# Optimization experiments

Hardware: AMD Instinct MI355X
Metric: run time of the kernel (lower is better)

The kernel has to match this reference:

```python
import jax, jax.numpy as jnp
import numpy as np

H = 8          # heads
D = 512        # d_model
DK = D // H    # per-head dim
FF = 2048      # feed-forward size
STACKS = 3
VOCAB = 5000
PAD = 0
LN_EPS = 1e-6


def _layer_norm(x, g, b):
    mu = jnp.mean(x, axis=-1, keepdims=True)
    var = jnp.mean(jnp.square(x - mu), axis=-1, keepdims=True)
    return (x - mu) * jax.lax.rsqrt(var + LN_EPS) * g + b


def _positional_encoding(T, d):
    pos = jnp.arange(T, dtype=jnp.float32)[:, None]                      # (T,1)
    div = jnp.exp(jnp.arange(0, d, 2, dtype=jnp.float32) * (-np.log(10000.0) / d))
    pe = jnp.zeros((T, d), dtype=jnp.float32)
    pe = pe.at[:, 0::2].set(jnp.sin(pos * div))
    pe = pe.at[:, 1::2].set(jnp.cos(pos * div))
    return pe  # (T, D)


def _mha(q_in, kv, wq, bq, wk, bk, wv, bv, wo, bo, mask):
    B, Tq, _ = q_in.shape
    Tk = kv.shape[1]
    q = (q_in @ wq + bq).reshape(B, Tq, H, DK).transpose(0, 2, 1, 3)   # (B,H,Tq,DK)
    k = (kv @ wk + bk).reshape(B, Tk, H, DK).transpose(0, 2, 1, 3)
    v = (kv @ wv + bv).reshape(B, Tk, H, DK).transpose(0, 2, 1, 3)
    score = jnp.einsum('bhqd,bhkd->bhqk', q, k) / jnp.sqrt(jnp.float32(DK))
    if mask is not None:
        score = jnp.where(mask, score, jnp.float32(-1e9))
    p = jax.nn.softmax(score, axis=-1)
    out = jnp.einsum('bhqk,bhkd->bhqd', p, v)
    out = out.transpose(0, 2, 1, 3).reshape(B, Tq, D)
    return out @ wo + bo


def setup_inputs() -> dict:
    key = jax.random.key(0)
    ks = jax.random.split(key, 24)
    s = 0.02
    inp = {
        'target': jax.random.randint(ks[0], (32, 256), 0, VOCAB),
        'memory': jax.random.normal(ks[1], (32, 1024, D), dtype=jnp.float32),
        'emb': jax.random.normal(ks[2], (VOCAB, D), dtype=jnp.float32) * s,
        'ln_g': jnp.ones((D,), jnp.float32),
        'ln_b': jnp.zeros((D,), jnp.float32),
        'ff_w1': jax.random.normal(ks[3], (D, FF), jnp.float32) * s,
        'ff_b1': jnp.zeros((FF,), jnp.float32),
        'ff_w2': jax.random.normal(ks[4], (FF, D), jnp.float32) * s,
        'ff_b2': jnp.zeros((D,), jnp.float32),
    }
    names = ['wq', 'wk', 'wv', 'wo']
    for i, n in enumerate(names):
        inp['sa_' + n] = jax.random.normal(ks[5 + i], (D, D), jnp.float32) * s
        inp['sa_b' + n[1]] = jnp.zeros((D,), jnp.float32)
        inp['ca_' + n] = jax.random.normal(ks[9 + i], (D, D), jnp.float32) * s
        inp['ca_b' + n[1]] = jnp.zeros((D,), jnp.float32)
    return inp


def reference(target, memory, emb, ln_g, ln_b, ff_w1, ff_b1, ff_w2, ff_b2,
              sa_wq, sa_bq, sa_wk, sa_bk, sa_wv, sa_bv, sa_wo, sa_bo,
              ca_wq, ca_bq, ca_wk, ca_bk, ca_wv, ca_bv, ca_wo, ca_bo):
    B, T = target.shape
    x = emb[target] * jnp.sqrt(jnp.float32(D))              # (B,T,D)
    x = x + _positional_encoding(T, D)                       # dropout = identity (eval)
    # masks: causal & pad for self-attn; cross-attn mask is all-ones -> skip
    pad = (target != PAD)[:, None, :, None]                  # (B,1,T,1)
    causal = jnp.tril(jnp.ones((T, T), dtype=bool))          # (T,T)
    tgt_mask = pad & causal                                  # (B,1,T,T)
    out = x
    for _ in range(STACKS):  # shared parameters
        n = _layer_norm(out, ln_g, ln_b)
        out = out + _mha(n, n, sa_wq, sa_bq, sa_wk, sa_bk, sa_wv, sa_bv, sa_wo, sa_bo, tgt_mask)
        n = _layer_norm(out, ln_g, ln_b)
        out = out + _mha(n, memory, ca_wq, ca_bq, ca_wk, ca_bk, ca_wv, ca_bv, ca_wo, ca_bo, None)
        n = _layer_norm(out, ln_g, ln_b)
        out = out + (jax.nn.relu(n @ ff_w1 + ff_b1) @ ff_w2 + ff_b2)
    return _layer_norm(out, ln_g, ln_b)
```

## Files before the change

### kernel.cpp

```cpp
#include <hip/hip_runtime.h>
#include <cstdint>
#include <cstddef>

typedef unsigned short u16;
typedef __bf16 bf16x8 __attribute__((ext_vector_type(8)));
typedef float f32x4 __attribute__((ext_vector_type(4)));

#define DEV static __device__ __forceinline__

#define QSCALE 0.18033688011112042f

DEV u16 f2bf(float f) { unsigned v; __builtin_memcpy(&v, &f, 4); v += 0x7fffu + ((v >> 16) & 1u); return (u16)(v >> 16); }

DEV void gll16(const void* g, void* l) {
    __builtin_amdgcn_global_load_lds(
        (__attribute__((address_space(1))) void*)g,
        (__attribute__((address_space(3))) void*)l, 16, 0, 0);
}

__global__ void embed_pe(const int* __restrict__ tgt, const float* __restrict__ emb,
                         float* __restrict__ x)
{
    const int bt = blockIdx.x;
    const int t  = bt & 255;
    const int tok = tgt[bt];
    for (int d = threadIdx.x; d < 512; d += 256) {
        float e  = emb[(size_t)tok * 512 + d] * 22.62741699796952f;
        int   d0 = d & ~1;
        float ang = (float)t * expf((float)d0 * (-9.210340371976184f / 512.f));
        float pe  = (d & 1) ? cosf(ang) : sinf(ang);
        x[(size_t)bt * 512 + d] = e + pe;
    }
}

__global__ void transpose_k(const float* __restrict__ in, u16* __restrict__ out,
                            int K, int N)
{
    int id = blockIdx.x * 256 + threadIdx.x;
    int k = id / N, n = id % N;
    out[(size_t)n * K + k] = f2bf(in[id]);
}

__global__ void memcast(const float* __restrict__ in, u16* __restrict__ out)
{
    int i = (blockIdx.x * 256 + threadIdx.x) * 4;
    float4 v = *(const float4*)(in + i);
    uint2 w;
    w.x = (unsigned)f2bf(v.x) | ((unsigned)f2bf(v.y) << 16);
    w.y = (unsigned)f2bf(v.z) | ((unsigned)f2bf(v.w) << 16);
    *(uint2*)(out + i) = w;
}

__global__ void concat_bias(const float* __restrict__ a, const float* __restrict__ b,
                            float* __restrict__ out)
{
    int i = blockIdx.x * 256 + threadIdx.x;
    if (i < 512) { out[i] = a[i]; out[512 + i] = b[i]; }
}

template<bool OUTF32>
__global__ void layernorm_k(const float* __restrict__ x, const float* __restrict__ g,
                            const float* __restrict__ b, void* __restrict__ outv)
{
    const int row  = blockIdx.x * 4 + (threadIdx.x >> 6);
    const int lane = threadIdx.x & 63;
    const float* xr = x + (size_t)row * 512;
    float4 v0 = *(const float4*)(xr + lane * 4);
    float4 v1 = *(const float4*)(xr + 256 + lane * 4);
    float s = v0.x + v0.y + v0.z + v0.w + v1.x + v1.y + v1.z + v1.w;
    float q = v0.x*v0.x + v0.y*v0.y + v0.z*v0.z + v0.w*v0.w
            + v1.x*v1.x + v1.y*v1.y + v1.z*v1.z + v1.w*v1.w;
#pragma unroll
    for (int o = 1; o < 64; o <<= 1) { s += __shfl_xor(s, o, 64); q += __shfl_xor(q, o, 64); }
    float mu  = s * (1.f / 512.f);
    float var = q * (1.f / 512.f) - mu * mu;
    float rs  = rsqrtf(fmaxf(var, 0.f) + 1e-6f);

#pragma unroll
    for (int h = 0; h < 2; h++) {
        const int d0 = h * 256 + lane * 4;
        float4 v = h ? v1 : v0;
        float4 gg = *(const float4*)(g + d0);
        float4 bb = *(const float4*)(b + d0);
        float o0 = (v.x - mu) * rs * gg.x + bb.x;
        float o1 = (v.y - mu) * rs * gg.y + bb.y;
        float o2 = (v.z - mu) * rs * gg.z + bb.z;
        float o3 = (v.w - mu) * rs * gg.w + bb.w;
        if (OUTF32) {
            *(float4*)((float*)outv + (size_t)row * 512 + d0) = make_float4(o0, o1, o2, o3);
        } else {
            uint2 w;
            w.x = (unsigned)f2bf(o0) | ((unsigned)f2bf(o1) << 16);
            w.y = (unsigned)f2bf(o2) | ((unsigned)f2bf(o3) << 16);
            *(uint2*)((u16*)outv + (size_t)row * 512 + d0) = w;
        }
    }
}

template<int EPI, bool BROW, int BN, int QS>
__launch_bounds__(256, BN == 64 ? 4 : 2)
__global__ void gemm_bt(const u16* __restrict__ A, int lda,
                        const u16* __restrict__ Bt,
                        const float* __restrict__ bias,
                        void* __restrict__ outp, int ldo, int K)
{
    constexpr int NJ = BN / 32;
    __shared__ u16 As[128 * 32];
    __shared__ u16 Bs[BN * 32];
    const int tid  = threadIdx.x;
    const int lane = tid & 63;
    const int wave = tid >> 6;
    const int quad = lane >> 4, l16 = lane & 15;
    const int l4 = lane >> 2, c8 = (lane & 3) * 8;
    const int m0 = blockIdx.y * 128, n0 = blockIdx.x * BN;
    const int wm = (wave >> 1) * 64, wn = (wave & 1) * (BN / 2);

    f32x4 acc[4][NJ];
#pragma unroll
    for (int i = 0; i < 4; i++)
#pragma unroll
        for (int j = 0; j < NJ; j++) acc[i][j] = f32x4{0.f, 0.f, 0.f, 0.f};

    for (int k0 = 0; k0 < K; k0 += 32) {
        __syncthreads();
        gll16(&A[(size_t)(m0 + wave * 32 + l4)      * lda + k0 + c8], &As[(wave * 32) * 32]);
        gll16(&A[(size_t)(m0 + wave * 32 + 16 + l4) * lda + k0 + c8], &As[(wave * 32 + 16) * 32]);
        if (BN == 128) {
            gll16(&Bt[(size_t)(n0 + wave * 32 + l4)      * K + k0 + c8], &Bs[(wave * 32) * 32]);
            gll16(&Bt[(size_t)(n0 + wave * 32 + 16 + l4) * K + k0 + c8], &Bs[(wave * 32 + 16) * 32]);
        } else {
            gll16(&Bt[(size_t)(n0 + wave * 16 + l4) * K + k0 + c8], &Bs[(wave * 16) * 32]);
        }
        __syncthreads();
        bf16x8 af[4], bfr[NJ];
#pragma unroll
        for (int i = 0; i < 4; i++) af[i]  = *(const bf16x8*)&As[(wm + i * 16 + l16) * 32 + quad * 8];
#pragma unroll
        for (int j = 0; j < NJ; j++) bfr[j] = *(const bf16x8*)&Bs[(wn + j * 16 + l16) * 32 + quad * 8];
#pragma unroll
        for (int i = 0; i < 4; i++)
#pragma unroll
            for (int j = 0; j < NJ; j++)
                acc[i][j] = __builtin_amdgcn_mfma_f32_16x16x32_bf16(af[i], bfr[j], acc[i][j], 0, 0, 0);
    }

#pragma unroll
    for (int i = 0; i < 4; i++)
#pragma unroll
        for (int j = 0; j < NJ; j++) {
            const int col = n0 + wn + j * 16 + l16;
            const float bc = BROW ? 0.f : bias[col];
#pragma unroll
            for (int r = 0; r < 4; r++) {
                const int row = m0 + wm + i * 16 + quad * 4 + r;
                const float bv = BROW ? bias[row] : bc;
                float v = acc[i][j][r] + bv;
                if (QS == 1) v *= QSCALE;
                if (QS == 2 && col < 512) v *= QSCALE;
                if (EPI == 1) v = fmaxf(v, 0.f);
                if (EPI == 2) {
                    ((float*)outp)[(size_t)row * ldo + col] += v;
                } else {
                    ((u16*)outp)[(size_t)row * ldo + col] = f2bf(v);
                }
            }
        }
}

template<bool SELF>
__launch_bounds__(256, 4)
__global__ void attn(const u16* __restrict__ Qb, int qs,
                     const u16* __restrict__ Kb, int ks, int koff,
                     const u16* __restrict__ Vt, int ldv,
                     const int* __restrict__ target,
                     u16* __restrict__ Ob, int Tk)
{
    __shared__ u16 KsL[64 * 32], KsH[64 * 32];
    __shared__ u16 VsL[64 * 32], VsH[64 * 32];
    __shared__ float P32[4][16][68];
    __shared__ int needtail;
    const int tid  = threadIdx.x;
    const int lane = tid & 63;
    const int wave = tid >> 6;
    const int quad = lane >> 4, l16 = lane & 15;
    const int l4 = lane >> 2, c8 = (lane & 3) * 8;
    const int b = blockIdx.x, h = blockIdx.y, qz = blockIdx.z;
    const int qbase = qz * 64 + wave * 16;
    const int hq = h * 64;

    if (tid == 0) needtail = 0;

    const u16* qr = Qb + (size_t)(b * 256 + qbase + l16) * qs + hq;
    bf16x8 qf0 = *(const bf16x8*)(qr + quad * 8);
    bf16x8 qf1 = *(const bf16x8*)(qr + 32 + quad * 8);

    f32x4 o[4];
#pragma unroll
    for (int t = 0; t < 4; t++) o[t] = f32x4{0.f, 0.f, 0.f, 0.f};
    float ps = 0.f;
    bool rv[4];
    bool inv = false;
    if (SELF) {
#pragma unroll
        for (int r = 0; r < 4; r++) {
            rv[r] = (target[b * 256 + qbase + quad * 4 + r] != 0);
            inv |= !rv[r];
        }
    }
    const bool winv = SELF ? __any(inv) : false;
    __syncthreads();
    if (winv && lane == 0) needtail = 1;
    __syncthreads();
    const int nch = SELF ? (needtail ? (Tk >> 6) : (qz + 1)) : (Tk >> 6);

    const u16* kbase = Kb + (size_t)b * Tk * ks + koff + hq;
    const u16* vbase = Vt + (size_t)hq * ldv + (size_t)b * Tk;
    float* pw = &P32[wave][0][0];

    for (int c = 0; c < nch; c++) {
        const int k0 = c * 64;
        __syncthreads();
        gll16(kbase + (size_t)(k0 + wave * 16 + l4) * ks + c8,      &KsL[(wave * 16) * 32]);
        gll16(kbase + (size_t)(k0 + wave * 16 + l4) * ks + 32 + c8, &KsH[(wave * 16) * 32]);
        gll16(vbase + (size_t)(wave * 16 + l4) * ldv + k0 + c8,      &VsL[(wave * 16) * 32]);
        gll16(vbase + (size_t)(wave * 16 + l4) * ldv + k0 + 32 + c8, &VsH[(wave * 16) * 32]);
        __syncthreads();

        float s[4][4];
#pragma unroll
        for (int g = 0; g < 4; g++) {
            bf16x8 kf0 = *(const bf16x8*)&KsL[(g * 16 + l16) * 32 + quad * 8];
            bf16x8 kf1 = *(const bf16x8*)&KsH[(g * 16 + l16) * 32 + quad * 8];
            f32x4 sv = f32x4{0.f, 0.f, 0.f, 0.f};
            sv = __builtin_amdgcn_mfma_f32_16x16x32_bf16(qf0, kf0, sv, 0, 0, 0);
            sv = __builtin_amdgcn_mfma_f32_16x16x32_bf16(qf1, kf1, sv, 0, 0, 0);
#pragma unroll
            for (int r = 0; r < 4; r++) s[g][r] = sv[r];
        }
        if (SELF) {
            if (k0 + 64 > qbase) {
#pragma unroll
                for (int g = 0; g < 4; g++)
#pragma unroll
                    for (int r = 0; r < 4; r++)
                        if (k0 + g * 16 + l16 > qbase + quad * 4 + r) s[g][r] = -1e9f;
            }
            if (winv) {
#pragma unroll
                for (int g = 0; g < 4; g++)
#pragma unroll
                    for (int r = 0; r < 4; r++)
                        if (!rv[r]) s[g][r] = 0.f;
            }
        }
#pragma unroll
        for (int g = 0; g < 4; g++)
#pragma unroll
            for (int r = 0; r < 4; r++)
                pw[(quad * 4 + r) * 68 + g * 16 + l16] = s[g][r];
        f32x4 ra0 = *(const f32x4*)&pw[l16 * 68 + quad * 8];
        f32x4 ra1 = *(const f32x4*)&pw[l16 * 68 + quad * 8 + 4];
        f32x4 rb0 = *(const f32x4*)&pw[l16 * 68 + 32 + quad * 8];
        f32x4 rb1 = *(const f32x4*)&pw[l16 * 68 + 36 + quad * 8];
        bf16x8 pa0, pa1;
#pragma unroll
        for (int j = 0; j < 4; j++) { float p = exp2f(ra0[j]); ps += p; pa0[j]     = (__bf16)p; }
#pragma unroll
        for (int j = 0; j < 4; j++) { float p = exp2f(ra1[j]); ps += p; pa0[4 + j] = (__bf16)p; }
#pragma unroll
        for (int j = 0; j < 4; j++) { float p = exp2f(rb0[j]); ps += p; pa1[j]     = (__bf16)p; }
#pragma unroll
        for (int j = 0; j < 4; j++) { float p = exp2f(rb1[j]); ps += p; pa1[4 + j] = (__bf16)p; }
#pragma unroll
        for (int t = 0; t < 4; t++) {
            bf16x8 vf0 = *(const bf16x8*)&VsL[(t * 16 + l16) * 32 + quad * 8];
            bf16x8 vf1 = *(const bf16x8*)&VsH[(t * 16 + l16) * 32 + quad * 8];
            o[t] = __builtin_amdgcn_mfma_f32_16x16x32_bf16(pa0, vf0, o[t], 0, 0, 0);
            o[t] = __builtin_amdgcn_mfma_f32_16x16x32_bf16(pa1, vf1, o[t], 0, 0, 0);
        }
    }

    ps += __shfl_xor(ps, 16, 64);
    ps += __shfl_xor(ps, 32, 64);
#pragma unroll
    for (int r = 0; r < 4; r++) {
        const float inv_l = 1.f / __shfl(ps, quad * 4 + r, 64);
        const int tq = qbase + quad * 4 + r;
        u16* orow = Ob + (size_t)(b * 256 + tq) * 512 + hq;
#pragma unroll
        for (int t = 0; t < 4; t++) orow[t * 16 + l16] = f2bf(o[t][r] * inv_l);
    }
}

#define O_X      ((size_t)0)
#define O_N      ((size_t)16777216)
#define O_QK     ((size_t)25165824)
#define O_VTS    ((size_t)41943040)
#define O_ATT    ((size_t)50331648)
#define O_FFN    ((size_t)58720256)
#define O_KVC    ((size_t)92274688)
#define O_VTC    ((size_t)125829120)
#define O_WQKT   ((size_t)159383552)
#define O_SAVT   ((size_t)160432128)
#define O_WOT    ((size_t)160956416)
#define O_CAQT   ((size_t)161480704)
#define O_CAKT   ((size_t)162004992)
#define O_CAVT   ((size_t)162529280)
#define O_CAWOT  ((size_t)163053568)
#define O_FF1T   ((size_t)163577856)
#define O_FF2T   ((size_t)165675008)
#define O_BQK    ((size_t)167772160)

extern "C" void kernel_launch(void* const* d_in, const int* in_sizes, int n_in,
                              void* d_out, int out_size, void* d_ws, size_t ws_size,
                              hipStream_t stream)
{
    const int*   target = (const int*)d_in[0];
    const float* memory = (const float*)d_in[1];
    const float* emb    = (const float*)d_in[2];
    const float* ln_g   = (const float*)d_in[3];
    const float* ln_b   = (const float*)d_in[4];
    const float* ff_w1  = (const float*)d_in[5];
    const float* ff_b1  = (const float*)d_in[6];
    const float* ff_w2  = (const float*)d_in[7];
    const float* ff_b2  = (const float*)d_in[8];
    const float* sa_wq  = (const float*)d_in[9];
    const float* sa_bq  = (const float*)d_in[10];
    const float* ca_wq  = (const float*)d_in[11];
    const float* ca_bq  = (const float*)d_in[12];
    const float* sa_wk  = (const float*)d_in[13];
    const float* sa_bk  = (const float*)d_in[14];
    const float* ca_wk  = (const float*)d_in[15];
    const float* ca_bk  = (const float*)d_in[16];
    const float* sa_wv  = (const float*)d_in[17];
    const float* sa_bv  = (const float*)d_in[18];
    const float* ca_wv  = (const float*)d_in[19];
    const float* ca_bv  = (const float*)d_in[20];
    const float* sa_wo  = (const float*)d_in[21];
    const float* sa_bo  = (const float*)d_in[22];
    const float* ca_wo  = (const float*)d_in[23];
    const float* ca_bo  = (const float*)d_in[24];

    char* ws = (char*)d_ws;
    float* xf   = (float*)(ws + O_X);
    u16* nbuf   = (u16*)(ws + O_N);
    u16* qk     = (u16*)(ws + O_QK);
    u16* qbuf   = (u16*)(ws + O_QK);
    u16* vts    = (u16*)(ws + O_VTS);
    u16* att    = (u16*)(ws + O_ATT);
    u16* ffn    = (u16*)(ws + O_FFN);
    u16* membf  = (u16*)(ws + O_FFN);
    u16* kvc    = (u16*)(ws + O_KVC);
    u16* vtc    = (u16*)(ws + O_VTC);
    u16* wqkt   = (u16*)(ws + O_WQKT);
    u16* savt   = (u16*)(ws + O_SAVT);
    u16* wot    = (u16*)(ws + O_WOT);
    u16* caqt   = (u16*)(ws + O_CAQT);
    u16* cakt   = (u16*)(ws + O_CAKT);
    u16* cavt   = (u16*)(ws + O_CAVT);
    u16* cawot  = (u16*)(ws + O_CAWOT);
    u16* ff1t   = (u16*)(ws + O_FF1T);
    u16* ff2t   = (u16*)(ws + O_FF2T);
    float* bqk  = (float*)(ws + O_BQK);

    transpose_k<<<1024, 256, 0, stream>>>(sa_wq, wqkt,             512, 512);
    transpose_k<<<1024, 256, 0, stream>>>(sa_wk, wqkt + 512 * 512, 512, 512);
    transpose_k<<<1024, 256, 0, stream>>>(sa_wv, savt,  512, 512);
    transpose_k<<<1024, 256, 0, stream>>>(sa_wo, wot,   512, 512);
    transpose_k<<<1024, 256, 0, stream>>>(ca_wq, caqt,  512, 512);
    transpose_k<<<1024, 256, 0, stream>>>(ca_wk, cakt,  512, 512);
    transpose_k<<<1024, 256, 0, stream>>>(ca_wv, cavt,  512, 512);
    transpose_k<<<1024, 256, 0, stream>>>(ca_wo, cawot, 512, 512);
    transpose_k<<<4096, 256, 0, stream>>>(ff_w1, ff1t,  512, 2048);
    transpose_k<<<4096, 256, 0, stream>>>(ff_w2, ff2t, 2048, 512);
    concat_bias<<<2, 256, 0, stream>>>(sa_bq, sa_bk, bqk);

    embed_pe<<<8192, 256, 0, stream>>>(target, emb, xf);

    memcast<<<16384, 256, 0, stream>>>(memory, membf);
    gemm_bt<0, false, 128, 0><<<dim3(4, 256), 256, 0, stream>>>(membf, 512, cakt, ca_bk, kvc, 512, 512);
    gemm_bt<0, true,  128, 0><<<dim3(256, 4), 256, 0, stream>>>(cavt, 512, membf, ca_bv, vtc, 32768, 512);

    for (int s = 0; s < 3; s++) {
        layernorm_k<false><<<2048, 256, 0, stream>>>(xf, ln_g, ln_b, nbuf);
        gemm_bt<0, false, 128, 2><<<dim3(8, 64), 256, 0, stream>>>(nbuf, 512, wqkt, bqk, qk, 1024, 512);
        gemm_bt<0, true,  64,  0><<<dim3(128, 4), 256, 0, stream>>>(savt, 512, nbuf, sa_bv, vts, 8192, 512);
        attn<true><<<dim3(32, 8, 4), 256, 0, stream>>>(qk, 1024, qk, 1024, 512, vts, 8192, target, att, 256);
        gemm_bt<2, false, 64, 0><<<dim3(8, 64), 256, 0, stream>>>(att, 512, wot, sa_bo, xf, 512, 512);
        layernorm_k<false><<<2048, 256, 0, stream>>>(xf, ln_g, ln_b, nbuf);
        gemm_bt<0, false, 64, 1><<<dim3(8, 64), 256, 0, stream>>>(nbuf, 512, caqt, ca_bq, qbuf, 512, 512);
        attn<false><<<dim3(32, 8, 4), 256, 0, stream>>>(qbuf, 512, kvc, 512, 0, vtc, 32768, nullptr, att, 1024);
        gemm_bt<2, false, 64, 0><<<dim3(8, 64), 256, 0, stream>>>(att, 512, cawot, ca_bo, xf, 512, 512);
        layernorm_k<false><<<2048, 256, 0, stream>>>(xf, ln_g, ln_b, nbuf);
        gemm_bt<1, false, 128, 0><<<dim3(16, 64), 256, 0, stream>>>(nbuf, 512, ff1t, ff_b1, ffn, 2048, 512);
        gemm_bt<2, false, 64, 0><<<dim3(8, 64), 256, 0, stream>>>(ffn, 2048, ff2t, ff_b2, xf, 512, 2048);
    }

    layernorm_k<true><<<2048, 256, 0, stream>>>(xf, ln_g, ln_b, d_out);
}
```

Baseline: 960.1 us.

## Add split-K with atomic accumulation, XCD-aware block remap, and narrower GEMM tiles

Adds a SPLIT template parameter so the residual-accumulating GEMMs (output projections and FF2) split K across gridDim.z and combine partial sums into the fp32 residual with atomicAdd, adding bias only in the first split. Block indices are remapped so consecutive workgroups are spread across the eight XCDs. The QKV and FF1 GEMMs switch from 128- to 64-wide N tiles to launch more workgroups. The aim is more parallelism for small grids (512 blocks) on a many-CU GPU, at the cost of atomic traffic and nondeterministic summation order.

```diff
diff --git a/kernel.cpp b/kernel.cpp
--- a/kernel.cpp
+++ b/kernel.cpp
@@ -97,7 +97,7 @@
     }
 }
 
-template<int EPI, bool BROW, int BN, int QS>
+template<int EPI, bool BROW, int BN, int QS, int SPLIT>
 __launch_bounds__(256, BN == 64 ? 4 : 2)
 __global__ void gemm_bt(const u16* __restrict__ A, int lda,
                         const u16* __restrict__ Bt,
@@ -107,21 +107,34 @@
     constexpr int NJ = BN / 32;
     __shared__ u16 As[128 * 32];
     __shared__ u16 Bs[BN * 32];
+
+    const int gx = gridDim.x, gy = gridDim.y;
+    const int nwg = gx * gy * gridDim.z;
+    int lin = blockIdx.x + gx * (blockIdx.y + gy * blockIdx.z);
+    lin = (lin & 7) * (nwg >> 3) + (lin >> 3);
+    const int bx = lin % gx;
+    const int rem = lin / gx;
+    const int by = rem % gy;
+    const int bz = rem / gy;
+
     const int tid  = threadIdx.x;
     const int lane = tid & 63;
     const int wave = tid >> 6;
     const int quad = lane >> 4, l16 = lane & 15;
     const int l4 = lane >> 2, c8 = (lane & 3) * 8;
-    const int m0 = blockIdx.y * 128, n0 = blockIdx.x * BN;
+    const int m0 = by * 128, n0 = bx * BN;
     const int wm = (wave >> 1) * 64, wn = (wave & 1) * (BN / 2);
 
+    const int kc = K / SPLIT;
+    const int kbeg = bz * kc;
+
     f32x4 acc[4][NJ];
 #pragma unroll
     for (int i = 0; i < 4; i++)
 #pragma unroll
         for (int j = 0; j < NJ; j++) acc[i][j] = f32x4{0.f, 0.f, 0.f, 0.f};
 
-    for (int k0 = 0; k0 < K; k0 += 32) {
+    for (int k0 = kbeg; k0 < kbeg + kc; k0 += 32) {
         __syncthreads();
         gll16(&A[(size_t)(m0 + wave * 32 + l4)      * lda + k0 + c8], &As[(wave * 32) * 32]);
         gll16(&A[(size_t)(m0 + wave * 32 + 16 + l4) * lda + k0 + c8], &As[(wave * 32 + 16) * 32]);
@@ -144,22 +157,24 @@
                 acc[i][j] = __builtin_amdgcn_mfma_f32_16x16x32_bf16(af[i], bfr[j], acc[i][j], 0, 0, 0);
     }
 
+    const bool dobias = (SPLIT == 1) || (bz == 0);
 #pragma unroll
     for (int i = 0; i < 4; i++)
 #pragma unroll
         for (int j = 0; j < NJ; j++) {
             const int col = n0 + wn + j * 16 + l16;
-            const float bc = BROW ? 0.f : bias[col];
+            const float bc = BROW ? 0.f : (dobias ? bias[col] : 0.f);
 #pragma unroll
             for (int r = 0; r < 4; r++) {
                 const int row = m0 + wm + i * 16 + quad * 4 + r;
-                const float bv = BROW ? bias[row] : bc;
+                const float bv = BROW ? (dobias ? bias[row] : 0.f) : bc;
                 float v = acc[i][j][r] + bv;
                 if (QS == 1) v *= QSCALE;
                 if (QS == 2 && col < 512) v *= QSCALE;
                 if (EPI == 1) v = fmaxf(v, 0.f);
                 if (EPI == 2) {
-                    ((float*)outp)[(size_t)row * ldo + col] += v;
+                    if (SPLIT > 1) atomicAdd((float*)outp + (size_t)row * ldo + col, v);
+                    else           ((float*)outp)[(size_t)row * ldo + col] += v;
                 } else {
                     ((u16*)outp)[(size_t)row * ldo + col] = f2bf(v);
                 }
@@ -378,22 +393,22 @@
     embed_pe<<<8192, 256, 0, stream>>>(target, emb, xf);
 
     memcast<<<16384, 256, 0, stream>>>(memory, membf);
-    gemm_bt<0, false, 128, 0><<<dim3(4, 256), 256, 0, stream>>>(membf, 512, cakt, ca_bk, kvc, 512, 512);
-    gemm_bt<0, true,  128, 0><<<dim3(256, 4), 256, 0, stream>>>(cavt, 512, membf, ca_bv, vtc, 32768, 512);
+    gemm_bt<0, false, 128, 0, 1><<<dim3(4, 256), 256, 0, stream>>>(membf, 512, cakt, ca_bk, kvc, 512, 512);
+    gemm_bt<0, true,  128, 0, 1><<<dim3(256, 4), 256, 0, stream>>>(cavt, 512, membf, ca_bv, vtc, 32768, 512);
 
     for (int s = 0; s < 3; s++) {
         layernorm_k<false><<<2048, 256, 0, stream>>>(xf, ln_g, ln_b, nbuf);
-        gemm_bt<0, false, 128, 2><<<dim3(8, 64), 256, 0, stream>>>(nbuf, 512, wqkt, bqk, qk, 1024, 512);
-        gemm_bt<0, true,  64,  0><<<dim3(128, 4), 256, 0, stream>>>(savt, 512, nbuf, sa_bv, vts, 8192, 512);
+        gemm_bt<0, false, 64, 2, 1><<<dim3(16, 64), 256, 0, stream>>>(nbuf, 512, wqkt, bqk, qk, 1024, 512);
+        gemm_bt<0, true,  64, 0, 1><<<dim3(128, 4), 256, 0, stream>>>(savt, 512, nbuf, sa_bv, vts, 8192, 512);
         attn<true><<<dim3(32, 8, 4), 256, 0, stream>>>(qk, 1024, qk, 1024, 512, vts, 8192, target, att, 256);
-        gemm_bt<2, false, 64, 0><<<dim3(8, 64), 256, 0, stream>>>(att, 512, wot, sa_bo, xf, 512, 512);
+        gemm_bt<2, false, 64, 0, 2><<<dim3(8, 64, 2), 256, 0, stream>>>(att, 512, wot, sa_bo, xf, 512, 512);
         layernorm_k<false><<<2048, 256, 0, stream>>>(xf, ln_g, ln_b, nbuf);
-        gemm_bt<0, false, 64, 1><<<dim3(8, 64), 256, 0, stream>>>(nbuf, 512, caqt, ca_bq, qbuf, 512, 512);
+        gemm_bt<0, false, 64, 1, 1><<<dim3(8, 64), 256, 0, stream>>>(nbuf, 512, caqt, ca_bq, qbuf, 512, 512);
         attn<false><<<dim3(32, 8, 4), 256, 0, stream>>>(qbuf, 512, kvc, 512, 0, vtc, 32768, nullptr, att, 1024);
-        gemm_bt<2, false, 64, 0><<<dim3(8, 64), 256, 0, stream>>>(att, 512, cawot, ca_bo, xf, 512, 512);
+        gemm_bt<2, false, 64, 0, 2><<<dim3(8, 64, 2), 256, 0, stream>>>(att, 512, cawot, ca_bo, xf, 512, 512);
         layernorm_k<false><<<2048, 256, 0, stream>>>(xf, ln_g, ln_b, nbuf);
-        gemm_bt<1, false, 128, 0><<<dim3(16, 64), 256, 0, stream>>>(nbuf, 512, ff1t, ff_b1, ffn, 2048, 512);
-        gemm_bt<2, false, 64, 0><<<dim3(8, 64), 256, 0, stream>>>(ffn, 2048, ff2t, ff_b2, xf, 512, 2048);
+        gemm_bt<1, false, 64, 0, 1><<<dim3(32, 64), 256, 0, stream>>>(nbuf, 512, ff1t, ff_b1, ffn, 2048, 512);
+        gemm_bt<2, false, 64, 0, 4><<<dim3(8, 64, 4), 256, 0, stream>>>(ffn, 2048, ff2t, ff_b2, xf, 512, 2048);
     }
 
     layernorm_k<true><<<2048, 256, 0, stream>>>(xf, ln_g, ln_b, d_out);
```

After: 1.091 ms. +13.6%, slower.
